# Kernel optimization log

Measured on AMD Instinct MI355X. Metric: run time of the kernel, lower is better.

Reference implementation:

```python
import jax, jax.numpy as jnp
import numpy as np

RANK = 16
ALPHA = 16.0
SCALING = ALPHA / RANK
N_ADAPTERS = 8
IN_F = 4096
OUT_F = 4096
BATCH = 4
SEQ = 2048


def setup_inputs() -> dict:
    key = jax.random.key(0)
    kx, ka, kb, ki = jax.random.split(key, 4)
    x = jax.random.normal(kx, (BATCH, SEQ, IN_F), dtype=jnp.float32)
    # A init: randn * 0.02 (as in module). B is zeros in the module; use small
    # random values here so the baseline output/grads are non-trivial.
    A = jax.random.normal(ka, (N_ADAPTERS, OUT_F, RANK), dtype=jnp.float32) * 0.02
    B = jax.random.normal(kb, (N_ADAPTERS, RANK, IN_F), dtype=jnp.float32) * 0.02
    adapter_ids = jax.random.randint(ki, (BATCH,), 0, N_ADAPTERS, dtype=jnp.int32)
    return {"x": x, "A": A, "B": B, "adapter_ids": adapter_ids}


def reference(x, A, B, adapter_ids):
    # Original: Bx = einsum('bni,ari->bnar', x, B); res = einsum('bnar,aor->bnao', Bx, A)
    # then res[arange(b), :, adapter_ids] * scaling.
    # Equivalent (gather-then-batched-GEMM): select each batch element's adapter
    # first, avoiding the O(n_adapters) dense intermediate. Same math.
    B_sel = B[adapter_ids]            # [b, r, in]
    A_sel = A[adapter_ids]            # [b, out, r]
    Bx = jnp.einsum('bni,bri->bnr', x, B_sel)   # [b, n, r]
    out = jnp.einsum('bnr,bor->bno', Bx, A_sel)  # [b, n, out]
    return out * SCALING
```

## Files before the change

kernel.cpp:

```cpp
#include <hip/hip_runtime.h>
#include <hip/hip_bf16.h>

#define RANK   16
#define IN_F   4096
#define OUT_F  4096
#define NROWS  8192

typedef __bf16 bf16x8   __attribute__((ext_vector_type(8)));
typedef float  floatx4  __attribute__((ext_vector_type(4)));

__device__ __bf16 g_bx[NROWS * RANK];

static __device__ __forceinline__ bf16x8 cvt8(floatx4 a, floatx4 b) {
    bf16x8 r;
    r[0] = (__bf16)a[0]; r[1] = (__bf16)a[1]; r[2] = (__bf16)a[2]; r[3] = (__bf16)a[3];
    r[4] = (__bf16)b[0]; r[5] = (__bf16)b[1]; r[6] = (__bf16)b[2]; r[7] = (__bf16)b[3];
    return r;
}

__global__ __launch_bounds__(512, 4) void
lora_bx_kernel(const float* __restrict__ x, const float* __restrict__ Bw,
               const int* __restrict__ ids)
{
    const int tile = blockIdx.x;
    const int row0 = tile * 16;
    const int adapter = ids[row0 >> 11];
    const int tid  = threadIdx.x;
    const int wave = tid >> 6;
    const int lane = tid & 63;

    __shared__ float red[8][256];

    const int m    = lane & 15;
    const int quad = lane >> 4;
    const int k0   = wave * 512 + quad * 8;
    const float* xp = x + (size_t)(row0 + m) * IN_F + k0;
    const float* bp = Bw + (size_t)adapter * (RANK * IN_F) + m * IN_F + k0;

    floatx4 acc = {0.f, 0.f, 0.f, 0.f};
#pragma unroll
    for (int s = 0; s < 16; ++s) {
        floatx4 xa = *reinterpret_cast<const floatx4*>(xp + s * 32);
        floatx4 xb = *reinterpret_cast<const floatx4*>(xp + s * 32 + 4);
        floatx4 ba = *reinterpret_cast<const floatx4*>(bp + s * 32);
        floatx4 bb = *reinterpret_cast<const floatx4*>(bp + s * 32 + 4);
        acc = __builtin_amdgcn_mfma_f32_16x16x32_bf16(
            cvt8(xa, xb), cvt8(ba, bb), acc, 0, 0, 0);
    }
#pragma unroll
    for (int j = 0; j < 4; ++j)
        red[wave][(quad * 4 + j) * 16 + m] = acc[j];
    __syncthreads();
    if (tid < 256) {
        float s = ((red[0][tid] + red[1][tid]) + (red[2][tid] + red[3][tid]))
                + ((red[4][tid] + red[5][tid]) + (red[6][tid] + red[7][tid]));
        g_bx[tile * 256 + tid] = (__bf16)s;
    }
}

__global__ __launch_bounds__(256, 8) void
lora_out_kernel(const float* __restrict__ Aw, const int* __restrict__ ids,
                float* __restrict__ out)
{
    const int blk      = blockIdx.x;
    const int row_tile = blk >> 2;
    const int ochunk   = blk & 3;
    const int row0     = row_tile * 16;
    const int adapter  = ids[row0 >> 11];
    const int tid  = threadIdx.x;
    const int wave = tid >> 6;
    const int lane = tid & 63;
    const int rl   = lane & 15;
    const int quad = lane >> 4;

    bf16x8 zfrag;
#pragma unroll
    for (int i = 0; i < 8; ++i) zfrag[i] = (__bf16)0.f;

    bf16x8 bfrag = zfrag;
    if (quad < 2)
        bfrag = *reinterpret_cast<const bf16x8*>(g_bx + row0 * 16 + rl * 16 + quad * 8);

    const float* ap = Aw + (size_t)adapter * (OUT_F * RANK);
    const int o_base = ochunk * 1024 + wave * 256;

#pragma unroll 4
    for (int t = 0; t < 16; ++t) {
        const int o0 = o_base + t * 16;
        bf16x8 afrag = zfrag;
        if (quad < 2) {
            floatx4 fa = *reinterpret_cast<const floatx4*>(
                ap + (size_t)(o0 + rl) * RANK + quad * 8);
            floatx4 fb = *reinterpret_cast<const floatx4*>(
                ap + (size_t)(o0 + rl) * RANK + quad * 8 + 4);
            afrag = cvt8(fa, fb);
        }
        floatx4 c = {0.f, 0.f, 0.f, 0.f};
        c = __builtin_amdgcn_mfma_f32_16x16x32_bf16(afrag, bfrag, c, 0, 0, 0);
        *reinterpret_cast<floatx4*>(
            out + (size_t)(row0 + rl) * OUT_F + o0 + quad * 4) = c;
    }
}

extern "C" void kernel_launch(void* const* d_in, const int* in_sizes, int n_in,
                              void* d_out, int out_size, void* d_ws, size_t ws_size,
                              hipStream_t stream) {
    const float* x   = (const float*)d_in[0];
    const float* Aw  = (const float*)d_in[1];
    const float* Bw  = (const float*)d_in[2];
    const int*   ids = (const int*)d_in[3];
    float* out = (float*)d_out;

    lora_bx_kernel<<<dim3(NROWS / 16), dim3(512), 0, stream>>>(x, Bw, ids);
    lora_out_kernel<<<dim3(2048), dim3(256), 0, stream>>>(Aw, ids, out);
}
```

Before: 283.9 us.

## Split Bx reduction over K across blocks with fp32 partials and prefetch

Splits the x·B^T reduction across four blocks per 16-row tile, each of 256 threads covering a quarter of K. Partial sums go to a global fp32 buffer that the output kernel adds up before converting to bf16. The inner loop also software-prefetches the next x and B slices. This raises the block count and memory-level parallelism for the x read, which dominates the first kernel. The cost is extra global traffic for the partials and four reads per row in the second kernel.

```diff
diff --git a/kernel.cpp b/kernel.cpp
--- a/kernel.cpp
+++ b/kernel.cpp
@@ -5,11 +5,12 @@
 #define IN_F   4096
 #define OUT_F  4096
 #define NROWS  8192
+#define KSPLIT 4
 
 typedef __bf16 bf16x8   __attribute__((ext_vector_type(8)));
 typedef float  floatx4  __attribute__((ext_vector_type(4)));
 
-__device__ __bf16 g_bx[NROWS * RANK];
+__device__ float g_part[KSPLIT * NROWS * RANK];
 
 static __device__ __forceinline__ bf16x8 cvt8(floatx4 a, floatx4 b) {
     bf16x8 r;
@@ -18,44 +19,51 @@
     return r;
 }
 
-__global__ __launch_bounds__(512, 4) void
+__global__ __launch_bounds__(256, 8) void
 lora_bx_kernel(const float* __restrict__ x, const float* __restrict__ Bw,
                const int* __restrict__ ids)
 {
-    const int tile = blockIdx.x;
-    const int row0 = tile * 16;
+    const int blk  = blockIdx.x;
+    const int rt   = blk >> 2;
+    const int kq   = blk & 3;
+    const int row0 = rt * 16;
     const int adapter = ids[row0 >> 11];
     const int tid  = threadIdx.x;
     const int wave = tid >> 6;
     const int lane = tid & 63;
 
-    __shared__ float red[8][256];
+    __shared__ float red[4][256];
 
     const int m    = lane & 15;
     const int quad = lane >> 4;
-    const int k0   = wave * 512 + quad * 8;
+    const int k0   = kq * 1024 + wave * 256 + quad * 8;
     const float* xp = x + (size_t)(row0 + m) * IN_F + k0;
     const float* bp = Bw + (size_t)adapter * (RANK * IN_F) + m * IN_F + k0;
 
     floatx4 acc = {0.f, 0.f, 0.f, 0.f};
+    floatx4 xa = *reinterpret_cast<const floatx4*>(xp);
+    floatx4 xb = *reinterpret_cast<const floatx4*>(xp + 4);
+    floatx4 ba = *reinterpret_cast<const floatx4*>(bp);
+    floatx4 bb = *reinterpret_cast<const floatx4*>(bp + 4);
 #pragma unroll
-    for (int s = 0; s < 16; ++s) {
-        floatx4 xa = *reinterpret_cast<const floatx4*>(xp + s * 32);
-        floatx4 xb = *reinterpret_cast<const floatx4*>(xp + s * 32 + 4);
-        floatx4 ba = *reinterpret_cast<const floatx4*>(bp + s * 32);
-        floatx4 bb = *reinterpret_cast<const floatx4*>(bp + s * 32 + 4);
+    for (int s = 0; s < 8; ++s) {
+        floatx4 xa2, xb2, ba2, bb2;
+        if (s < 7) {
+            xa2 = *reinterpret_cast<const floatx4*>(xp + (s + 1) * 32);
+            xb2 = *reinterpret_cast<const floatx4*>(xp + (s + 1) * 32 + 4);
+            ba2 = *reinterpret_cast<const floatx4*>(bp + (s + 1) * 32);
+            bb2 = *reinterpret_cast<const floatx4*>(bp + (s + 1) * 32 + 4);
+        }
         acc = __builtin_amdgcn_mfma_f32_16x16x32_bf16(
             cvt8(xa, xb), cvt8(ba, bb), acc, 0, 0, 0);
+        xa = xa2; xb = xb2; ba = ba2; bb = bb2;
     }
 #pragma unroll
     for (int j = 0; j < 4; ++j)
         red[wave][(quad * 4 + j) * 16 + m] = acc[j];
     __syncthreads();
-    if (tid < 256) {
-        float s = ((red[0][tid] + red[1][tid]) + (red[2][tid] + red[3][tid]))
-                + ((red[4][tid] + red[5][tid]) + (red[6][tid] + red[7][tid]));
-        g_bx[tile * 256 + tid] = (__bf16)s;
-    }
+    const float s = (red[0][tid] + red[1][tid]) + (red[2][tid] + red[3][tid]);
+    g_part[((size_t)kq * NROWS + row0) * RANK + tid] = s;
 }
 
 __global__ __launch_bounds__(256, 8) void
@@ -78,8 +86,16 @@
     for (int i = 0; i < 8; ++i) zfrag[i] = (__bf16)0.f;
 
     bf16x8 bfrag = zfrag;
-    if (quad < 2)
-        bfrag = *reinterpret_cast<const bf16x8*>(g_bx + row0 * 16 + rl * 16 + quad * 8);
+    if (quad < 2) {
+        const float* pp = g_part + ((size_t)(row0 + rl)) * RANK + quad * 8;
+        floatx4 s0 = {0.f, 0.f, 0.f, 0.f}, s1 = {0.f, 0.f, 0.f, 0.f};
+#pragma unroll
+        for (int p = 0; p < KSPLIT; ++p) {
+            s0 += *reinterpret_cast<const floatx4*>(pp + (size_t)p * NROWS * RANK);
+            s1 += *reinterpret_cast<const floatx4*>(pp + (size_t)p * NROWS * RANK + 4);
+        }
+        bfrag = cvt8(s0, s1);
+    }
 
     const float* ap = Aw + (size_t)adapter * (OUT_F * RANK);
     const int o_base = ochunk * 1024 + wave * 256;
@@ -111,6 +127,6 @@
     const int*   ids = (const int*)d_in[3];
     float* out = (float*)d_out;
 
-    lora_bx_kernel<<<dim3(NROWS / 16), dim3(512), 0, stream>>>(x, Bw, ids);
+    lora_bx_kernel<<<dim3(NROWS / 16 * KSPLIT), dim3(256), 0, stream>>>(x, Bw, ids);
     lora_out_kernel<<<dim3(2048), dim3(256), 0, stream>>>(Aw, ids, out);
 }
```

After: 283.3 us. About the same (-0.2%).

## Replace MFMA output GEMM with register-cached fp32 FMA over 32-row tiles

Applied to the files above, without the earlier changes.

The second kernel is rewritten so each thread keeps four output columns' worth of A rows (64 floats) in registers. It then loops over 32 rows, reading the fp32 Bx row (a broadcast load) and computing the rank-16 dot products with scalar FMAs, writing one contiguous float4 per row. This removes the half-empty MFMA fragments and repeated A loads per 16-row tile, and keeps Bx in fp32 instead of bf16. The cost is more VALU work, higher register pressure, fewer blocks, and double-sized Bx scratch traffic. Output stores stay coalesced.

```diff
diff --git a/kernel.cpp b/kernel.cpp
--- a/kernel.cpp
+++ b/kernel.cpp
@@ -6,10 +6,10 @@
 #define OUT_F  4096
 #define NROWS  8192
 
-typedef __bf16 bf16x8   __attribute__((ext_vector_type(8)));
-typedef float  floatx4  __attribute__((ext_vector_type(4)));
+typedef __bf16 bf16x8  __attribute__((ext_vector_type(8)));
+typedef float  floatx4 __attribute__((ext_vector_type(4)));
 
-__device__ __bf16 g_bx[NROWS * RANK];
+__device__ float g_bx[NROWS * RANK];
 
 static __device__ __forceinline__ bf16x8 cvt8(floatx4 a, floatx4 b) {
     bf16x8 r;
@@ -54,51 +54,50 @@
     if (tid < 256) {
         float s = ((red[0][tid] + red[1][tid]) + (red[2][tid] + red[3][tid]))
                 + ((red[4][tid] + red[5][tid]) + (red[6][tid] + red[7][tid]));
-        g_bx[tile * 256 + tid] = (__bf16)s;
+        g_bx[tile * 256 + tid] = s;
     }
 }
 
-__global__ __launch_bounds__(256, 8) void
+__global__ __launch_bounds__(256, 4) void
 lora_out_kernel(const float* __restrict__ Aw, const int* __restrict__ ids,
                 float* __restrict__ out)
 {
-    const int blk      = blockIdx.x;
-    const int row_tile = blk >> 2;
-    const int ochunk   = blk & 3;
-    const int row0     = row_tile * 16;
-    const int adapter  = ids[row0 >> 11];
+    const int b    = blockIdx.x;
+    const int cc   = b & 3;
+    const int rg   = b >> 2;
+    const int row0 = rg * 32;
+    const int adapter = ids[row0 >> 11];
     const int tid  = threadIdx.x;
     const int wave = tid >> 6;
     const int lane = tid & 63;
-    const int rl   = lane & 15;
-    const int quad = lane >> 4;
+    const int c0   = cc * 1024 + wave * 256 + lane * 4;
 
-    bf16x8 zfrag;
+    const float* ap = Aw + ((size_t)adapter * OUT_F + c0) * RANK;
+    floatx4 a[16];
 #pragma unroll
-    for (int i = 0; i < 8; ++i) zfrag[i] = (__bf16)0.f;
+    for (int i = 0; i < 16; ++i)
+        a[i] = *reinterpret_cast<const floatx4*>(ap + i * 4);
 
-    bf16x8 bfrag = zfrag;
-    if (quad < 2)
-        bfrag = *reinterpret_cast<const bf16x8*>(g_bx + row0 * 16 + rl * 16 + quad * 8);
-
-    const float* ap = Aw + (size_t)adapter * (OUT_F * RANK);
-    const int o_base = ochunk * 1024 + wave * 256;
-
-#pragma unroll 4
-    for (int t = 0; t < 16; ++t) {
-        const int o0 = o_base + t * 16;
-        bf16x8 afrag = zfrag;
-        if (quad < 2) {
-            floatx4 fa = *reinterpret_cast<const floatx4*>(
-                ap + (size_t)(o0 + rl) * RANK + quad * 8);
-            floatx4 fb = *reinterpret_cast<const floatx4*>(
-                ap + (size_t)(o0 + rl) * RANK + quad * 8 + 4);
-            afrag = cvt8(fa, fb);
+#pragma unroll 2
+    for (int rr = 0; rr < 32; ++rr) {
+        const int row = row0 + rr;
+        const float* bp = g_bx + (size_t)row * RANK;
+        const floatx4 b0 = *reinterpret_cast<const floatx4*>(bp);
+        const floatx4 b1 = *reinterpret_cast<const floatx4*>(bp + 4);
+        const floatx4 b2 = *reinterpret_cast<const floatx4*>(bp + 8);
+        const floatx4 b3 = *reinterpret_cast<const floatx4*>(bp + 12);
+        floatx4 ov;
+#pragma unroll
+        for (int j = 0; j < 4; ++j) {
+            const floatx4 a0 = a[j * 4 + 0], a1 = a[j * 4 + 1];
+            const floatx4 a2 = a[j * 4 + 2], a3 = a[j * 4 + 3];
+            float s = a0[0] * b0[0] + a0[1] * b0[1] + a0[2] * b0[2] + a0[3] * b0[3]
+                    + a1[0] * b1[0] + a1[1] * b1[1] + a1[2] * b1[2] + a1[3] * b1[3]
+                    + a2[0] * b2[0] + a2[1] * b2[1] + a2[2] * b2[2] + a2[3] * b2[3]
+                    + a3[0] * b3[0] + a3[1] * b3[1] + a3[2] * b3[2] + a3[3] * b3[3];
+            ov[j] = s;
         }
-        floatx4 c = {0.f, 0.f, 0.f, 0.f};
-        c = __builtin_amdgcn_mfma_f32_16x16x32_bf16(afrag, bfrag, c, 0, 0, 0);
-        *reinterpret_cast<floatx4*>(
-            out + (size_t)(row0 + rl) * OUT_F + o0 + quad * 4) = c;
+        *reinterpret_cast<floatx4*>(out + (size_t)row * OUT_F + c0) = ov;
     }
 }
 
@@ -111,6 +110,6 @@
     const int*   ids = (const int*)d_in[3];
     float* out = (float*)d_out;
 
-    lora_bx_kernel<<<dim3(NROWS / 16), dim3(512), 0, stream>>>(x, Bw, ids);
-    lora_out_kernel<<<dim3(2048), dim3(256), 0, stream>>>(Aw, ids, out);
+    lora_bx_kernel <<<dim3(NROWS / 16), dim3(512), 0, stream>>>(x, Bw, ids);
+    lora_out_kernel<<<dim3(1024),       dim3(256), 0, stream>>>(Aw, ids, out);
 }
```

Result: faster. 253.1 us (-10.8%).
